# Performance work log

Measured on AMD Instinct MI355X. Metric: run time of the kernel, lower is better.

## Reference

```python
import jax, jax.numpy as jnp
import numpy as np

N_LAYERS = 6
N_HEADS = 8
HIDDEN = 512
FILTER = 2048
KSIZE = 3
WINDOW = 10
DK = HIDDEN // N_HEADS


def _rel_to_abs(x):
    # x: [b, h, l, 2l-1] -> [b, h, l, l]
    b, h, l, _ = x.shape
    x = jnp.pad(x, ((0, 0), (0, 0), (0, 0), (0, 1)))
    x = x.reshape(b, h, l * 2 * l)
    x = jnp.pad(x, ((0, 0), (0, 0), (0, l - 1)))
    return x.reshape(b, h, l + 1, 2 * l - 1)[:, :, :l, l - 1:]


def _abs_to_rel(x):
    # x: [b, h, l, l] -> [b, h, l, 2l-1]
    b, h, l, _ = x.shape
    x = jnp.pad(x, ((0, 0), (0, 0), (0, 0), (0, l - 1)))
    x = x.reshape(b, h, l * l + l * (l - 1))
    x = jnp.pad(x, ((0, 0), (0, 0), (l, 0)))
    return x.reshape(b, h, l, 2 * l)[:, :, :, 1:]


def _get_rel_emb(emb, length):
    # emb: [1, 2w+1, dk] -> [1, 2*length-1, dk]  (static python ints)
    pad = max(length - (WINDOW + 1), 0)
    s = max(WINDOW + 1 - length, 0)
    e = s + 2 * length - 1
    emb = jnp.pad(emb, ((0, 0), (pad, pad), (0, 0)))
    return emb[:, s:e]


def _conv1x1(x, w, b):
    # x: [B, Cin, T], w: [Cout, Cin] -> [B, Cout, T]
    return jnp.einsum('oc,bct->bot', w, x) + b[None, :, None]


def _conv1d_same(x, w, b):
    # x: [B, Cin, T], w: [Cout, Cin, K], same padding (pad_l=(K-1)//2, pad_r=K//2)
    x = jnp.pad(x, ((0, 0), (0, 0), ((KSIZE - 1) // 2, KSIZE // 2)))
    y = jax.lax.conv_general_dilated(x, w, (1,), 'VALID',
                                     dimension_numbers=('NCH', 'OIH', 'NCH'))
    return y + b[None, :, None]


def _layer_norm(x, g, b):
    # normalize over channel axis (axis=1), eps=1e-5 (VITS LayerNorm)
    m = jnp.mean(x, axis=1, keepdims=True)
    v = jnp.var(x, axis=1, keepdims=True)
    return (x - m) * jax.lax.rsqrt(v + 1e-5) * g[None, :, None] + b[None, :, None]


def _mha(x, attn_mask, Wq, bq, Wk, bk, Wv, bv, Wo, bo, erk, erv):
    B, C, T = x.shape
    q = _conv1x1(x, Wq, bq)
    k = _conv1x1(x, Wk, bk)
    v = _conv1x1(x, Wv, bv)
    # [B, C, T] -> [B, H, T, Dk]
    def split_heads(t):
        return t.reshape(B, N_HEADS, DK, T).transpose(0, 1, 3, 2)
    q, k, v = split_heads(q), split_heads(k), split_heads(v)
    scale = 1.0 / np.sqrt(DK).astype(np.float32)
    scores = jnp.einsum('bhtd,bhsd->bhts', q * scale, k)
    # relative position logits
    rel_k = _get_rel_emb(erk, T)[0]                       # [2T-1, Dk]
    rel_logits = jnp.einsum('bhtd,rd->bhtr', q * scale, rel_k)
    scores = scores + _rel_to_abs(rel_logits)
    scores = jnp.where(attn_mask == 0, -1e4, scores)
    p = jax.nn.softmax(scores, axis=-1)
    out = jnp.einsum('bhts,bhsd->bhtd', p, v)
    rel_v = _get_rel_emb(erv, T)[0]                       # [2T-1, Dk]
    out = out + jnp.einsum('bhtr,rd->bhtd', _abs_to_rel(p), rel_v)
    out = out.transpose(0, 1, 3, 2).reshape(B, C, T)
    return _conv1x1(out, Wo, bo)


def _ffn(x, x_mask, W1, bf1, W2, bf2):
    y = _conv1d_same(x * x_mask, W1, bf1)
    y = jax.nn.relu(y)
    y = _conv1d_same(y * x_mask, W2, bf2)
    return y * x_mask


def reference(x, x_mask, Wq, bq, Wk, bk, Wv, bv, Wo, bo, erk, erv,
              g1, b1, g2, b2, W1, bf1, W2, bf2):
    attn_mask = x_mask[:, :, None, :] * x_mask[:, :, :, None]  # [B,1,T,T]
    x = x * x_mask
    for i in range(N_LAYERS):
        y = _mha(x, attn_mask, Wq[i], bq[i], Wk[i], bk[i], Wv[i], bv[i],
                 Wo[i], bo[i], erk[i], erv[i])
        x = _layer_norm(x + y, g1[i], b1[i])
        y = _ffn(x, x_mask, W1[i], bf1[i], W2[i], bf2[i])
        x = _layer_norm(x + y, g2[i], b2[i])
    return x * x_mask


def setup_inputs() -> dict:
    key = jax.random.key(0)
    ks = jax.random.split(key, 20)
    B, T = 8, 512
    xavier = lambda k, sh, fan: jax.random.normal(k, sh, jnp.float32) * np.sqrt(2.0 / fan).astype(np.float32)
    rel_std = DK ** -0.5
    return {
        'x': jax.random.normal(ks[0], (B, HIDDEN, T), jnp.float32),
        'x_mask': jnp.ones((B, 1, T), jnp.float32),
        'Wq': xavier(ks[1], (N_LAYERS, HIDDEN, HIDDEN), 2 * HIDDEN),
        'bq': jnp.zeros((N_LAYERS, HIDDEN), jnp.float32),
        'Wk': xavier(ks[2], (N_LAYERS, HIDDEN, HIDDEN), 2 * HIDDEN),
        'bk': jnp.zeros((N_LAYERS, HIDDEN), jnp.float32),
        'Wv': xavier(ks[3], (N_LAYERS, HIDDEN, HIDDEN), 2 * HIDDEN),
        'bv': jnp.zeros((N_LAYERS, HIDDEN), jnp.float32),
        'Wo': xavier(ks[4], (N_LAYERS, HIDDEN, HIDDEN), 2 * HIDDEN),
        'bo': jnp.zeros((N_LAYERS, HIDDEN), jnp.float32),
        'erk': jax.random.normal(ks[5], (N_LAYERS, 1, 2 * WINDOW + 1, DK), jnp.float32) * rel_std,
        'erv': jax.random.normal(ks[6], (N_LAYERS, 1, 2 * WINDOW + 1, DK), jnp.float32) * rel_std,
        'g1': jnp.ones((N_LAYERS, HIDDEN), jnp.float32),
        'b1': jnp.zeros((N_LAYERS, HIDDEN), jnp.float32),
        'g2': jnp.ones((N_LAYERS, HIDDEN), jnp.float32),
        'b2': jnp.zeros((N_LAYERS, HIDDEN), jnp.float32),
        'W1': jax.random.normal(ks[7], (N_LAYERS, FILTER, HIDDEN, KSIZE), jnp.float32) * np.sqrt(1.0 / (HIDDEN * KSIZE)).astype(np.float32),
        'bf1': jnp.zeros((N_LAYERS, FILTER), jnp.float32),
        'W2': jax.random.normal(ks[8], (N_LAYERS, HIDDEN, FILTER, KSIZE), jnp.float32) * np.sqrt(1.0 / (FILTER * KSIZE)).astype(np.float32),
        'bf2': jnp.zeros((N_LAYERS, HIDDEN), jnp.float32),
    }
```

## Files before the change

kernel.cpp:

```cpp
#include <hip/hip_runtime.h>


#define NLAYERS 6
#define BB 8
#define TT 512
#define CC 512
#define FF 2048
#define HH 8
#define DKK 64
#define WW 10

static_assert(CC == HH * DKK, "");

typedef __attribute__((ext_vector_type(8))) short short8;
typedef __attribute__((ext_vector_type(4))) float f32x4;
typedef unsigned short ushort;

#define BCTS ((size_t)BB * CC * TT)

__device__ __forceinline__ ushort f2bs(float f) {
    unsigned u = __float_as_uint(f);
    u = (u + 0x7FFFu + ((u >> 16) & 1u)) >> 16;
    return (ushort)u;
}
__device__ __forceinline__ float bf2f(ushort u) {
    return __uint_as_float(((unsigned)u) << 16);
}
__device__ __forceinline__ float wave_sum(float v) {
    #pragma unroll
    for (int off = 32; off > 0; off >>= 1) v += __shfl_xor(v, off, 64);
    return v;
}

__global__ __launch_bounds__(256) void init_trans(const float* __restrict__ in,
                                                  const float* __restrict__ mask,
                                                  float* __restrict__ xf,
                                                  ushort* __restrict__ xt) {
    __shared__ float tile[32][33];
    const int t0 = blockIdx.x * 32;
    const int c0 = blockIdx.y * 32;
    const int b = blockIdx.z;
    const int col = threadIdx.x & 31;
    const int row = threadIdx.x >> 5;
    const float* src = in + ((size_t)b * CC + c0) * TT + t0;
    #pragma unroll
    for (int r = 0; r < 32; r += 8)
        tile[row + r][col] = src[(size_t)(row + r) * TT + col];
    __syncthreads();
    #pragma unroll
    for (int r = 0; r < 32; r += 8) {
        const int t = t0 + row + r;
        const float mv = mask[b * TT + t];
        const float v = tile[col][row + r] * mv;
        const size_t idx = ((size_t)(b * TT) + t) * CC + c0 + col;
        xf[idx] = v;
        xt[idx] = f2bs(v);
    }
}

__global__ __launch_bounds__(256) void final_kernel(const float* __restrict__ xf,
                                                    const float* __restrict__ mask,
                                                    float* __restrict__ out) {
    __shared__ float tile[32][33];
    const int t0 = blockIdx.x * 32;
    const int c0 = blockIdx.y * 32;
    const int b = blockIdx.z;
    const int col = threadIdx.x & 31;
    const int row = threadIdx.x >> 5;
    #pragma unroll
    for (int r = 0; r < 32; r += 8)
        tile[row + r][col] = xf[((size_t)(b * TT) + t0 + row + r) * CC + c0 + col];
    __syncthreads();
    #pragma unroll
    for (int r = 0; r < 32; r += 8) {
        const int c = c0 + row + r;
        const int t = t0 + col;
        out[((size_t)b * CC + c) * TT + t] = tile[col][row + r] * mask[b * TT + t];
    }
}

__global__ __launch_bounds__(256) void wcvt_layer(const float* __restrict__ Wq,
                                                  const float* __restrict__ Wk,
                                                  const float* __restrict__ Wv,
                                                  const float* __restrict__ bq,
                                                  const float* __restrict__ bk,
                                                  const float* __restrict__ bv,
                                                  const float* __restrict__ Wo,
                                                  const float* __restrict__ W1,
                                                  const float* __restrict__ W2,
                                                  ushort* __restrict__ Wqkv,
                                                  float* __restrict__ bqkv,
                                                  ushort* __restrict__ Wot,
                                                  ushort* __restrict__ W1t,
                                                  ushort* __restrict__ W2t) {
    size_t i = (size_t)blockIdx.x * 256 + threadIdx.x;
    if (i < 1536)
        bqkv[i] = (i < 512) ? bq[i] : (i < 1024) ? bk[i - 512] : bv[i - 1024];
    if (i < 786432) {
        const int o = (int)(i >> 9), c = (int)(i & 511);
        const float* src = (o < 512) ? Wq : (o < 1024) ? Wk : Wv;
        Wqkv[i] = f2bs(src[(size_t)(o & 511) * 512 + c]);
        return;
    }
    i -= 786432;
    if (i < 262144) { Wot[i] = f2bs(Wo[i]); return; }
    i -= 262144;
    if (i < 3145728) {
        const int c = (int)(i & 511);
        const int o = (int)((i >> 9) & 2047);
        const int tap = (int)(i >> 20);
        W1t[i] = f2bs(W1[((size_t)o * 512 + c) * 3 + tap]);
        return;
    }
    i -= 3145728;
    if (i < 3145728) {
        const int c = (int)(i & 2047);
        const int o = (int)((i >> 11) & 511);
        const int tap = (int)(i >> 20);
        W2t[i] = f2bs(W2[((size_t)o * 2048 + c) * 3 + tap]);
    }
}

template <int MODE, int TN>
__global__ __launch_bounds__(256) void gemm128(const ushort* __restrict__ Wt,
                                               const float* __restrict__ bias,
                                               const ushort* __restrict__ Xin,
                                               void* __restrict__ Out,
                                               const float* __restrict__ mask,
                                               int O, int K, int taps, int kcs) {
    const int blk = blockIdx.x;
    const int b = blk >> 2;
    const int t0 = (blk & 3) * 128;
    const int o0 = blockIdx.y * TN;
    const int tid = threadIdx.x;
    const int wid = tid >> 6, lane = tid & 63, ln = lane & 15, q = lane >> 4;
    constexpr int MF = (TN == 128) ? 4 : 2;
    const int msub = (TN == 128) ? (wid & 1) * 64 : wid * 32;
    const int nsub = (TN == 128) ? (wid >> 1) * 64 : 0;

    __shared__ ushort Xs[128][40];
    __shared__ ushort Ws[TN][40];

    f32x4 acc[MF][4] = {};

    const int KC = K >> 5;
    const int NI = taps * KC;
    const int kcm = KC - 1;

    const int rx = tid >> 1;
    const int cx = (tid & 1) << 4;
    const int rw = (TN == 128) ? (tid >> 1) : (tid >> 2);
    const int cw = (TN == 128) ? ((tid & 1) << 4) : ((tid & 3) << 3);

    uint4 xr0, xr1, wr0, wr1;
    const uint4 zero = make_uint4(0u, 0u, 0u, 0u);

    auto load = [&](int it) {
        const int tap = it >> kcs;
        const int c0 = (it & kcm) << 5;
        const int shift = (taps > 1) ? (tap - 1) : 0;
        const int tt = t0 + rx + shift;
        const bool okt = (tt >= 0) && (tt < TT);
        const ushort* xp = Xin + ((size_t)(b * TT + (okt ? tt : 0)) * K + c0 + cx);
        xr0 = okt ? *(const uint4*)xp : zero;
        xr1 = okt ? *(const uint4*)(xp + 8) : zero;
        const ushort* wp = Wt + ((size_t)(tap * O + o0 + rw) * K + c0 + cw);
        wr0 = *(const uint4*)wp;
        if (TN == 128) wr1 = *(const uint4*)(wp + 8);
    };

    load(0);
    for (int it = 0; it < NI; ++it) {
        __syncthreads();
        *(uint4*)&Xs[rx][cx] = xr0;
        *(uint4*)&Xs[rx][cx + 8] = xr1;
        *(uint4*)&Ws[rw][cw] = wr0;
        if (TN == 128) *(uint4*)&Ws[rw][cw + 8] = wr1;
        if (it + 1 < NI) load(it + 1);
        __syncthreads();
        short8 afr[MF], bfr[4];
        #pragma unroll
        for (int mi = 0; mi < MF; ++mi)
            afr[mi] = *(const short8*)&Xs[msub + mi * 16 + ln][q * 8];
        #pragma unroll
        for (int ni = 0; ni < 4; ++ni)
            bfr[ni] = *(const short8*)&Ws[nsub + ni * 16 + ln][q * 8];
        #pragma unroll
        for (int mi = 0; mi < MF; ++mi)
            #pragma unroll
            for (int ni = 0; ni < 4; ++ni)
                acc[mi][ni] = __builtin_amdgcn_mfma_f32_16x16x32_bf16(
                    afr[mi], bfr[ni], acc[mi][ni], 0, 0, 0);
    }

    #pragma unroll
    for (int ni = 0; ni < 4; ++ni) {
        const int o = o0 + nsub + ni * 16 + ln;
        const float bv = bias[o];
        #pragma unroll
        for (int mi = 0; mi < MF; ++mi) {
            const int t = t0 + msub + mi * 16 + q * 4;
            if (MODE == 0) {
                float* Op = (float*)Out;
                #pragma unroll
                for (int r = 0; r < 4; ++r)
                    Op[((size_t)(b * TT) + t + r) * O + o] = acc[mi][ni][r] + bv;
            } else {
                ushort* Op = (ushort*)Out;
                const int which = o >> 9, oo = o & 511;
                if (which < 2) {
                    #pragma unroll
                    for (int r = 0; r < 4; ++r)
                        Op[(size_t)which * BCTS + ((size_t)(b * TT) + t + r) * CC + oo] =
                            f2bs(acc[mi][ni][r] + bv);
                } else {
                    ushort tmp[4];
                    #pragma unroll
                    for (int r = 0; r < 4; ++r) tmp[r] = f2bs(acc[mi][ni][r] + bv);
                    *(uint2*)&Op[2 * BCTS + ((size_t)(b * CC) + oo) * TT + t] =
                        *(const uint2*)tmp;
                }
            }
        }
    }
}

template <int TN, int KSPLIT, int MODE>
__global__ __launch_bounds__(256) void conv_gemm(const ushort* __restrict__ Wt,
                                                 const float* __restrict__ bias,
                                                 const ushort* __restrict__ Xin,
                                                 void* __restrict__ Out,
                                                 const float* __restrict__ mask,
                                                 int O, int K) {
    const int blk = blockIdx.x;
    const int b = blk >> 2;
    const int t0 = (blk & 3) * 128;
    const int o0 = blockIdx.y * TN;
    const int kz = (KSPLIT > 1) ? blockIdx.z : 0;
    const int tid = threadIdx.x;
    const int wid = tid >> 6, lane = tid & 63, ln = lane & 15, q = lane >> 4;
    constexpr int MF = (TN == 128) ? 4 : 2;
    constexpr int TSH = (TN == 128) ? 7 : 6;
    const int msub = (TN == 128) ? (wid & 1) * 64 : wid * 32;
    const int nsub = (TN == 128) ? (wid >> 1) * 64 : 0;

    __shared__ ushort Xs[130][40];
    __shared__ ushort Ws[3 * TN][40];

    f32x4 acc[MF][4] = {};

    const int Kc = K / KSPLIT;
    const int cbase = kz * Kc;
    const int NC = Kc >> 5;

    const int rx = tid >> 1;
    const int cx = (tid & 1) << 4;
    const int rw0 = tid >> 2;
    const int cw = (tid & 3) << 3;

    const ushort* Xb = Xin + (size_t)b * TT * K;

    for (int cc = 0; cc < NC; ++cc) {
        const int c0 = cbase + (cc << 5);
        __syncthreads();
        {
            const ushort* xp = Xb + (size_t)(t0 + rx) * K + c0 + cx;
            *(uint4*)&Xs[rx + 1][cx] = *(const uint4*)xp;
            *(uint4*)&Xs[rx + 1][cx + 8] = *(const uint4*)(xp + 8);
        }
        if (tid < 8) {
            const int hr = (tid < 4) ? -1 : 128;
            const int cu = (tid & 3) << 3;
            const int tg = t0 + hr;
            uint4 v = make_uint4(0u, 0u, 0u, 0u);
            if (tg >= 0 && tg < TT)
                v = *(const uint4*)(Xb + (size_t)tg * K + c0 + cu);
            *(uint4*)&Xs[hr + 1][cu] = v;
        }
        #pragma unroll
        for (int j = 0; j < 3 * TN / 64; ++j) {
            const int r = rw0 + j * 64;
            const int tap = r >> TSH, o = r & (TN - 1);
            const ushort* wp = Wt + ((size_t)(tap * O + o0 + o)) * K + c0 + cw;
            *(uint4*)&Ws[r][cw] = *(const uint4*)wp;
        }
        __syncthreads();
        #pragma unroll
        for (int tap = 0; tap < 3; ++tap) {
            short8 afr[MF], bfr[4];
            #pragma unroll
            for (int mi = 0; mi < MF; ++mi)
                afr[mi] = *(const short8*)&Xs[msub + mi * 16 + ln + tap][q * 8];
            #pragma unroll
            for (int ni = 0; ni < 4; ++ni)
                bfr[ni] = *(const short8*)&Ws[tap * TN + nsub + ni * 16 + ln][q * 8];
            #pragma unroll
            for (int mi = 0; mi < MF; ++mi)
                #pragma unroll
                for (int ni = 0; ni < 4; ++ni)
                    acc[mi][ni] = __builtin_amdgcn_mfma_f32_16x16x32_bf16(
                        afr[mi], bfr[ni], acc[mi][ni], 0, 0, 0);
        }
    }

    #pragma unroll
    for (int ni = 0; ni < 4; ++ni) {
        const int o = o0 + nsub + ni * 16 + ln;
        #pragma unroll
        for (int mi = 0; mi < MF; ++mi) {
            const int t = t0 + msub + mi * 16 + q * 4;
            if (MODE == 1) {
                const float bv = bias[o];
                ushort* Op = (ushort*)Out;
                #pragma unroll
                for (int r = 0; r < 4; ++r) {
                    float v = fmaxf(acc[mi][ni][r] + bv, 0.f) * mask[b * TT + t + r];
                    Op[((size_t)(b * TT) + t + r) * (size_t)O + o] = f2bs(v);
                }
            } else {
                float* Op = (float*)Out + (size_t)kz * BCTS;
                #pragma unroll
                for (int r = 0; r < 4; ++r)
                    Op[((size_t)(b * TT) + t + r) * O + o] = acc[mi][ni][r];
            }
        }
    }
}

__global__ __launch_bounds__(256) void fattn_kernel(const ushort* __restrict__ qkvt,
                                                    const float* __restrict__ mask,
                                                    const float* __restrict__ erk,
                                                    const float* __restrict__ erv,
                                                    ushort* __restrict__ xto) {
    const int tid = threadIdx.x;
    const int wm = tid >> 6;
    const int lane = tid & 63;
    const int ln = lane & 15;
    const int q4 = lane >> 4;
    const int bh = blockIdx.y;
    const int b = bh >> 3, h = bh & 7;
    const int t0g = blockIdx.x * 64 + wm * 16;

    __shared__ float ervs[2 * WW + 1][DKK];
    __shared__ float msS[TT];
    __shared__ float relS[4][16][22];
    __shared__ float band[4][16][24];
    __shared__ ushort Pt[4][16][40];

    for (int i = tid; i < (2 * WW + 1) * DKK; i += 256)
        ervs[i / DKK][i % DKK] = erv[i];
    for (int i = tid; i < TT; i += 256)
        msS[i] = mask[b * TT + i];

    #pragma unroll
    for (int i = 0; i < 6; ++i) {
        const int idx = lane + i * 64;
        ((float*)band[wm])[idx] = -1e30f;
    }

    const ushort* qrow = qkvt + ((size_t)(b * TT + t0g + ln) * CC + h * DKK);
    const short8 qb0 = *(const short8*)(qrow + q4 * 8);
    const short8 qb1 = *(const short8*)(qrow + 32 + q4 * 8);

    {
        const float* ekL = erk;
        short8 ea0, ea1;
        {
            const float* ep = ekL + ln * DKK + q4 * 8;
            #pragma unroll
            for (int j = 0; j < 8; ++j) ea0[j] = (short)f2bs(ep[j]);
            #pragma unroll
            for (int j = 0; j < 8; ++j) ea1[j] = (short)f2bs(ep[32 + j]);
        }
        f32x4 c0 = {};
        c0 = __builtin_amdgcn_mfma_f32_16x16x32_bf16(ea0, qb0, c0, 0, 0, 0);
        c0 = __builtin_amdgcn_mfma_f32_16x16x32_bf16(ea1, qb1, c0, 0, 0, 0);
        #pragma unroll
        for (int r = 0; r < 4; ++r)
            relS[wm][ln][q4 * 4 + r] = c0[r] * 0.125f;
        short8 eb0 = {}, eb1 = {};
        if (ln < 2 * WW + 1 - 16) {
            const float* ep = ekL + (16 + ln) * DKK + q4 * 8;
            #pragma unroll
            for (int j = 0; j < 8; ++j) eb0[j] = (short)f2bs(ep[j]);
            #pragma unroll
            for (int j = 0; j < 8; ++j) eb1[j] = (short)f2bs(ep[32 + j]);
        }
        f32x4 c1 = {};
        c1 = __builtin_amdgcn_mfma_f32_16x16x32_bf16(eb0, qb0, c1, 0, 0, 0);
        c1 = __builtin_amdgcn_mfma_f32_16x16x32_bf16(eb1, qb1, c1, 0, 0, 0);
        #pragma unroll
        for (int r = 0; r < 4; ++r) {
            const int w = 16 + q4 * 4 + r;
            if (w < 2 * WW + 1) relS[wm][ln][w] = c1[r] * 0.125f;
        }
    }

    __syncthreads();

    const float mt = msS[t0g + ln];

    float m_run = -1e30f, l_run = 0.f;
    f32x4 Oacc[4] = {};

    const ushort* Kbase = qkvt + BCTS + ((size_t)(b * TT) * CC + h * DKK);
    const ushort* Vbase = qkvt + 2 * BCTS + ((size_t)(b * CC + h * DKK) * TT);

    for (int s0 = 0; s0 < TT; s0 += 32) {
        const ushort* klo = Kbase + (size_t)(s0 + ln) * CC;
        const ushort* khi = klo + 16 * CC;
        const short8 ka0 = *(const short8*)(klo + q4 * 8);
        const short8 ka1 = *(const short8*)(klo + 32 + q4 * 8);
        const short8 kb0 = *(const short8*)(khi + q4 * 8);
        const short8 kb1 = *(const short8*)(khi + 32 + q4 * 8);

        f32x4 slo = {}, shi = {};
        slo = __builtin_amdgcn_mfma_f32_16x16x32_bf16(ka0, qb0, slo, 0, 0, 0);
        slo = __builtin_amdgcn_mfma_f32_16x16x32_bf16(ka1, qb1, slo, 0, 0, 0);
        shi = __builtin_amdgcn_mfma_f32_16x16x32_bf16(kb0, qb0, shi, 0, 0, 0);
        shi = __builtin_amdgcn_mfma_f32_16x16x32_bf16(kb1, qb1, shi, 0, 0, 0);

        float v[2][4];
        float bmax = -1e30f;
        const int tg = t0g + ln;
        #pragma unroll
        for (int half = 0; half < 2; ++half) {
            #pragma unroll
            for (int r = 0; r < 4; ++r) {
                const int s = s0 + half * 16 + q4 * 4 + r;
                const int wb = s - tg + WW;
                float vv = (half ? shi[r] : slo[r]) * 0.125f;
                if ((unsigned)wb <= 2u * WW) vv += relS[wm][ln][wb];
                if (mt * msS[s] == 0.f) vv = -1e4f;
                if ((unsigned)wb <= 2u * WW) band[wm][ln][wb] = vv;
                v[half][r] = vv;
                bmax = fmaxf(bmax, vv);
            }
        }
        bmax = fmaxf(bmax, __shfl_xor(bmax, 16, 64));
        bmax = fmaxf(bmax, __shfl_xor(bmax, 32, 64));

        const float mnew = fmaxf(m_run, bmax);
        const float alpha = __expf(m_run - mnew);
        m_run = mnew;

        float rsum = 0.f;
        ushort pb[8];
        #pragma unroll
        for (int half = 0; half < 2; ++half)
            #pragma unroll
            for (int r = 0; r < 4; ++r) {
                const float p = __expf(v[half][r] - mnew);
                rsum += p;
                pb[half * 4 + r] = f2bs(p);
            }
        rsum += __shfl_xor(rsum, 16, 64);
        rsum += __shfl_xor(rsum, 32, 64);
        l_run = l_run * alpha + rsum;

        *(uint2*)&Pt[wm][ln][q4 * 4] = *(const uint2*)&pb[0];
        *(uint2*)&Pt[wm][ln][16 + q4 * 4] = *(const uint2*)&pb[4];

        #pragma unroll
        for (int r = 0; r < 4; ++r) {
            const float alr = __shfl(alpha, q4 * 4 + r, 64);
            #pragma unroll
            for (int dt = 0; dt < 4; ++dt) Oacc[dt][r] *= alr;
        }

        const short8 pa = *(const short8*)&Pt[wm][ln][q4 * 8];
        #pragma unroll
        for (int dt = 0; dt < 4; ++dt) {
            const short8 vb = *(const short8*)(Vbase + (size_t)(dt * 16 + ln) * TT + s0 + q4 * 8);
            Oacc[dt] = __builtin_amdgcn_mfma_f32_16x16x32_bf16(pa, vb, Oacc[dt], 0, 0, 0);
        }
    }

    float mr[4], invl[4];
    #pragma unroll
    for (int r = 0; r < 4; ++r) {
        mr[r] = __shfl(m_run, q4 * 4 + r, 64);
        invl[r] = 1.f / __shfl(l_run, q4 * 4 + r, 64);
    }
    f32x4 racc[4] = {};
    for (int w = 0; w <= 2 * WW; ++w) {
        float ev[4];
        #pragma unroll
        for (int dt = 0; dt < 4; ++dt) ev[dt] = ervs[w][dt * 16 + ln];
        #pragma unroll
        for (int r = 0; r < 4; ++r) {
            const float pw = __expf(band[wm][q4 * 4 + r][w] - mr[r]);
            #pragma unroll
            for (int dt = 0; dt < 4; ++dt) racc[dt][r] += pw * ev[dt];
        }
    }
    #pragma unroll
    for (int r = 0; r < 4; ++r) {
        const int t = t0g + q4 * 4 + r;
        #pragma unroll
        for (int dt = 0; dt < 4; ++dt)
            xto[((size_t)(b * TT) + t) * CC + h * DKK + dt * 16 + ln] =
                f2bs((Oacc[dt][r] + racc[dt][r]) * invl[r]);
    }
}

__global__ __launch_bounds__(256) void addln_kernel(float* __restrict__ x,
                                                    const float* __restrict__ p0,
                                                    const float* __restrict__ p1,
                                                    const float* __restrict__ biasc,
                                                    const float* __restrict__ g,
                                                    const float* __restrict__ bt,
                                                    const float* __restrict__ mask,
                                                    int maskY,
                                                    ushort* __restrict__ xtout,
                                                    int maskOut) {
    const int row = blockIdx.x * 4 + (threadIdx.x >> 6);
    const int lane = threadIdx.x & 63;
    const float m = mask[row];
    const float mv = maskY ? m : 1.f;
    const float mo = maskOut ? m : 1.f;
    const size_t base = (size_t)row * CC;
    const int c0 = lane * 8;

    f32x4 v0, v1;
    {
        f32x4 a0 = *(const f32x4*)(x + base + c0);
        f32x4 a1 = *(const f32x4*)(x + base + c0 + 4);
        f32x4 y0 = *(const f32x4*)(p0 + base + c0);
        f32x4 y1 = *(const f32x4*)(p0 + base + c0 + 4);
        if (p1) {
            f32x4 z0 = *(const f32x4*)(p1 + base + c0);
            f32x4 z1 = *(const f32x4*)(p1 + base + c0 + 4);
            #pragma unroll
            for (int r = 0; r < 4; ++r) { y0[r] += z0[r]; y1[r] += z1[r]; }
        }
        if (biasc) {
            f32x4 bc0 = *(const f32x4*)(biasc + c0);
            f32x4 bc1 = *(const f32x4*)(biasc + c0 + 4);
            #pragma unroll
            for (int r = 0; r < 4; ++r) { y0[r] += bc0[r]; y1[r] += bc1[r]; }
        }
        #pragma unroll
        for (int r = 0; r < 4; ++r) {
            v0[r] = a0[r] + y0[r] * mv;
            v1[r] = a1[r] + y1[r] * mv;
        }
    }

    float s = 0.f, s2 = 0.f;
    #pragma unroll
    for (int r = 0; r < 4; ++r) {
        s += v0[r] + v1[r];
        s2 += v0[r] * v0[r] + v1[r] * v1[r];
    }
    s = wave_sum(s);
    s2 = wave_sum(s2);
    const float mean = s * (1.f / CC);
    const float var = s2 * (1.f / CC) - mean * mean;
    const float rstd = rsqrtf(var + 1e-5f);

    f32x4 g0 = *(const f32x4*)(g + c0);
    f32x4 g1v = *(const f32x4*)(g + c0 + 4);
    f32x4 bt0 = *(const f32x4*)(bt + c0);
    f32x4 bt1 = *(const f32x4*)(bt + c0 + 4);
    f32x4 o0, o1;
    ushort ob[8];
    #pragma unroll
    for (int r = 0; r < 4; ++r) {
        o0[r] = (v0[r] - mean) * rstd * g0[r] + bt0[r];
        o1[r] = (v1[r] - mean) * rstd * g1v[r] + bt1[r];
        ob[r] = f2bs(o0[r] * mo);
        ob[4 + r] = f2bs(o1[r] * mo);
    }
    *(f32x4*)(x + base + c0) = o0;
    *(f32x4*)(x + base + c0 + 4) = o1;
    *(uint4*)(xtout + base + c0) = *(const uint4*)ob;
}

extern "C" void kernel_launch(void* const* d_in, const int* in_sizes, int n_in,
                              void* d_out, int out_size, void* d_ws, size_t ws_size,
                              hipStream_t stream) {
    const float* x_in = (const float*)d_in[0];
    const float* mask = (const float*)d_in[1];
    const float* Wq = (const float*)d_in[2];
    const float* bq = (const float*)d_in[3];
    const float* Wk = (const float*)d_in[4];
    const float* bk = (const float*)d_in[5];
    const float* Wv = (const float*)d_in[6];
    const float* bv = (const float*)d_in[7];
    const float* Wo = (const float*)d_in[8];
    const float* bo = (const float*)d_in[9];
    const float* erk = (const float*)d_in[10];
    const float* erv = (const float*)d_in[11];
    const float* g1 = (const float*)d_in[12];
    const float* b1 = (const float*)d_in[13];
    const float* g2 = (const float*)d_in[14];
    const float* b2 = (const float*)d_in[15];
    const float* W1 = (const float*)d_in[16];
    const float* bf1 = (const float*)d_in[17];
    const float* W2 = (const float*)d_in[18];
    const float* bf2 = (const float*)d_in[19];

    float* xf = (float*)d_ws;
    ushort* Xt = (ushort*)(xf + BCTS);
    ushort* qkvt = Xt + BCTS;
    ushort* Xto = qkvt + 3 * BCTS;
    float* parts = (float*)(Xto + BCTS);
    ushort* Midt = (ushort*)(parts + 2 * BCTS);
    ushort* Wqkv = Midt + 4 * BCTS;
    float* bqkv = (float*)(Wqkv + (size_t)1536 * 512);
    ushort* Wot = (ushort*)(bqkv + 1536);
    ushort* W1t = Wot + (size_t)CC * CC;
    ushort* W2t = W1t + (size_t)3 * FF * CC;

    init_trans<<<dim3(TT / 32, CC / 32, BB), 256, 0, stream>>>(x_in, mask, xf, Xt);

    const size_t nW = 786432 + 262144 + 3145728 + 3145728;
    const int wcvtBlocks = (int)((nW + 255) / 256);

    for (int L = 0; L < NLAYERS; ++L) {
        wcvt_layer<<<wcvtBlocks, 256, 0, stream>>>(
            Wq + (size_t)L * CC * CC, Wk + (size_t)L * CC * CC, Wv + (size_t)L * CC * CC,
            bq + (size_t)L * CC, bk + (size_t)L * CC, bv + (size_t)L * CC,
            Wo + (size_t)L * CC * CC,
            W1 + (size_t)L * 3 * FF * CC, W2 + (size_t)L * 3 * FF * CC,
            Wqkv, bqkv, Wot, W1t, W2t);

        gemm128<2, 128><<<dim3(32, 12), 256, 0, stream>>>(
            Wqkv, bqkv, Xt, qkvt, mask, 1536, CC, 1, 4);

        fattn_kernel<<<dim3(TT / 64, BB * HH), 256, 0, stream>>>(
            qkvt, mask, erk + (size_t)L * (2 * WW + 1) * DKK,
            erv + (size_t)L * (2 * WW + 1) * DKK, Xto);

        gemm128<0, 64><<<dim3(32, 8), 256, 0, stream>>>(
            Wot, bo + (size_t)L * CC, Xto, parts, mask, CC, CC, 1, 4);
        addln_kernel<<<BB * TT / 4, 256, 0, stream>>>(
            xf, parts, nullptr, nullptr,
            g1 + (size_t)L * CC, b1 + (size_t)L * CC, mask, 0, Xt, 1);

        conv_gemm<128, 1, 1><<<dim3(32, FF / 128, 1), 256, 0, stream>>>(
            W1t, bf1 + (size_t)L * FF, Xt, Midt, mask, FF, CC);
        conv_gemm<64, 2, 3><<<dim3(32, CC / 64, 2), 256, 0, stream>>>(
            W2t, nullptr, Midt, parts, mask, CC, FF);
        addln_kernel<<<BB * TT / 4, 256, 0, stream>>>(
            xf, parts, parts + BCTS, bf2 + (size_t)L * CC,
            g2 + (size_t)L * CC, b2 + (size_t)L * CC, mask, 1, Xt, 0);
    }

    final_kernel<<<dim3(TT / 32, CC / 32, BB), 256, 0, stream>>>(xf, mask, (float*)d_out);
}
```

Baseline: 1.260 ms.

## Prefetch conv GEMM tiles into registers and rebalance split-K for FFN and output projection

The conv GEMM now loads the next K-chunk's activation and weight tiles into registers while the current chunk is computed from shared memory, so global loads overlap with MFMA work. The second FFN conv moves from 64-wide output tiles with 2-way split-K to 128-wide tiles with 4-way split-K, with the extra partial sums written into the idle QKV buffer. The attention output projection is also split 2-way over K, with its bias moved into the add+LayerNorm kernel, which now sums up to four partial buffers. This adds register pressure and extra fp32 partial-sum traffic in exchange for more parallelism and latency hiding.

```diff
diff --git a/kernel.cpp b/kernel.cpp
--- a/kernel.cpp
+++ b/kernel.cpp
@@ -127,11 +127,13 @@
                                                const ushort* __restrict__ Xin,
                                                void* __restrict__ Out,
                                                const float* __restrict__ mask,
-                                               int O, int K, int taps, int kcs) {
+                                               int O, int K, int taps, int kcs,
+                                               int ksp) {
     const int blk = blockIdx.x;
     const int b = blk >> 2;
     const int t0 = (blk & 3) * 128;
     const int o0 = blockIdx.y * TN;
+    const int kz = (MODE == 0) ? blockIdx.z : 0;
     const int tid = threadIdx.x;
     const int wid = tid >> 6, lane = tid & 63, ln = lane & 15, q = lane >> 4;
     constexpr int MF = (TN == 128) ? 4 : 2;
@@ -143,7 +145,9 @@
 
     f32x4 acc[MF][4] = {};
 
-    const int KC = K >> 5;
+    const int Kc = (MODE == 0) ? (K / ksp) : K;
+    const int cbase = kz * Kc;
+    const int KC = Kc >> 5;
     const int NI = taps * KC;
     const int kcm = KC - 1;
 
@@ -157,7 +161,7 @@
 
     auto load = [&](int it) {
         const int tap = it >> kcs;
-        const int c0 = (it & kcm) << 5;
+        const int c0 = cbase + ((it & kcm) << 5);
         const int shift = (taps > 1) ? (tap - 1) : 0;
         const int tt = t0 + rx + shift;
         const bool okt = (tt >= 0) && (tt < TT);
@@ -196,16 +200,16 @@
     #pragma unroll
     for (int ni = 0; ni < 4; ++ni) {
         const int o = o0 + nsub + ni * 16 + ln;
-        const float bv = bias[o];
         #pragma unroll
         for (int mi = 0; mi < MF; ++mi) {
             const int t = t0 + msub + mi * 16 + q * 4;
             if (MODE == 0) {
-                float* Op = (float*)Out;
+                float* Op = (float*)Out + (size_t)kz * BCTS;
                 #pragma unroll
                 for (int r = 0; r < 4; ++r)
-                    Op[((size_t)(b * TT) + t + r) * O + o] = acc[mi][ni][r] + bv;
+                    Op[((size_t)(b * TT) + t + r) * O + o] = acc[mi][ni][r];
             } else {
+                const float bv = bias[o];
                 ushort* Op = (ushort*)Out;
                 const int which = o >> 9, oo = o & 511;
                 if (which < 2) {
@@ -225,13 +229,15 @@
     }
 }
 
-template <int TN, int KSPLIT, int MODE>
+template <int KSPLIT, int MODE>
 __global__ __launch_bounds__(256) void conv_gemm(const ushort* __restrict__ Wt,
                                                  const float* __restrict__ bias,
                                                  const ushort* __restrict__ Xin,
                                                  void* __restrict__ Out,
+                                                 float* __restrict__ Out2,
                                                  const float* __restrict__ mask,
                                                  int O, int K) {
+    constexpr int TN = 128;
     const int blk = blockIdx.x;
     const int b = blk >> 2;
     const int t0 = (blk & 3) * 128;
@@ -239,15 +245,13 @@
     const int kz = (KSPLIT > 1) ? blockIdx.z : 0;
     const int tid = threadIdx.x;
     const int wid = tid >> 6, lane = tid & 63, ln = lane & 15, q = lane >> 4;
-    constexpr int MF = (TN == 128) ? 4 : 2;
-    constexpr int TSH = (TN == 128) ? 7 : 6;
-    const int msub = (TN == 128) ? (wid & 1) * 64 : wid * 32;
-    const int nsub = (TN == 128) ? (wid >> 1) * 64 : 0;
+    const int msub = (wid & 1) * 64;
+    const int nsub = (wid >> 1) * 64;
 
     __shared__ ushort Xs[130][40];
     __shared__ ushort Ws[3 * TN][40];
 
-    f32x4 acc[MF][4] = {};
+    f32x4 acc[4][4] = {};
 
     const int Kc = K / KSPLIT;
     const int cbase = kz * Kc;
@@ -260,42 +264,49 @@
 
     const ushort* Xb = Xin + (size_t)b * TT * K;
 
-    for (int cc = 0; cc < NC; ++cc) {
+    uint4 xr0, xr1, hx, wr[6];
+    auto load = [&](int cc) {
         const int c0 = cbase + (cc << 5);
-        __syncthreads();
-        {
-            const ushort* xp = Xb + (size_t)(t0 + rx) * K + c0 + cx;
-            *(uint4*)&Xs[rx + 1][cx] = *(const uint4*)xp;
-            *(uint4*)&Xs[rx + 1][cx + 8] = *(const uint4*)(xp + 8);
-        }
+        const ushort* xp = Xb + (size_t)(t0 + rx) * K + c0 + cx;
+        xr0 = *(const uint4*)xp;
+        xr1 = *(const uint4*)(xp + 8);
         if (tid < 8) {
             const int hr = (tid < 4) ? -1 : 128;
-            const int cu = (tid & 3) << 3;
             const int tg = t0 + hr;
-            uint4 v = make_uint4(0u, 0u, 0u, 0u);
+            hx = make_uint4(0u, 0u, 0u, 0u);
             if (tg >= 0 && tg < TT)
-                v = *(const uint4*)(Xb + (size_t)tg * K + c0 + cu);
-            *(uint4*)&Xs[hr + 1][cu] = v;
-        }
-        #pragma unroll
-        for (int j = 0; j < 3 * TN / 64; ++j) {
+                hx = *(const uint4*)(Xb + (size_t)tg * K + c0 + ((tid & 3) << 3));
+        }
+        #pragma unroll
+        for (int j = 0; j < 6; ++j) {
             const int r = rw0 + j * 64;
-            const int tap = r >> TSH, o = r & (TN - 1);
-            const ushort* wp = Wt + ((size_t)(tap * O + o0 + o)) * K + c0 + cw;
-            *(uint4*)&Ws[r][cw] = *(const uint4*)wp;
-        }
+            const int tap = r >> 7, o = r & (TN - 1);
+            wr[j] = *(const uint4*)(Wt + ((size_t)(tap * O + o0 + o)) * K + c0 + cw);
+        }
+    };
+
+    load(0);
+    for (int cc = 0; cc < NC; ++cc) {
         __syncthreads();
+        *(uint4*)&Xs[rx + 1][cx] = xr0;
+        *(uint4*)&Xs[rx + 1][cx + 8] = xr1;
+        if (tid < 8) *(uint4*)&Xs[(tid < 4) ? 0 : 129][(tid & 3) << 3] = hx;
+        #pragma unroll
+        for (int j = 0; j < 6; ++j)
+            *(uint4*)&Ws[rw0 + j * 64][cw] = wr[j];
+        if (cc + 1 < NC) load(cc + 1);
+        __syncthreads();
         #pragma unroll
         for (int tap = 0; tap < 3; ++tap) {
-            short8 afr[MF], bfr[4];
-            #pragma unroll
-            for (int mi = 0; mi < MF; ++mi)
+            short8 afr[4], bfr[4];
+            #pragma unroll
+            for (int mi = 0; mi < 4; ++mi)
                 afr[mi] = *(const short8*)&Xs[msub + mi * 16 + ln + tap][q * 8];
             #pragma unroll
             for (int ni = 0; ni < 4; ++ni)
                 bfr[ni] = *(const short8*)&Ws[tap * TN + nsub + ni * 16 + ln][q * 8];
             #pragma unroll
-            for (int mi = 0; mi < MF; ++mi)
+            for (int mi = 0; mi < 4; ++mi)
                 #pragma unroll
                 for (int ni = 0; ni < 4; ++ni)
                     acc[mi][ni] = __builtin_amdgcn_mfma_f32_16x16x32_bf16(
@@ -307,7 +318,7 @@
     for (int ni = 0; ni < 4; ++ni) {
         const int o = o0 + nsub + ni * 16 + ln;
         #pragma unroll
-        for (int mi = 0; mi < MF; ++mi) {
+        for (int mi = 0; mi < 4; ++mi) {
             const int t = t0 + msub + mi * 16 + q * 4;
             if (MODE == 1) {
                 const float bv = bias[o];
@@ -318,7 +329,8 @@
                     Op[((size_t)(b * TT) + t + r) * (size_t)O + o] = f2bs(v);
                 }
             } else {
-                float* Op = (float*)Out + (size_t)kz * BCTS;
+                float* Op = (kz < 2) ? ((float*)Out + (size_t)kz * BCTS)
+                                     : (Out2 + (size_t)(kz - 2) * BCTS);
                 #pragma unroll
                 for (int r = 0; r < 4; ++r)
                     Op[((size_t)(b * TT) + t + r) * O + o] = acc[mi][ni][r];
@@ -507,6 +519,8 @@
 __global__ __launch_bounds__(256) void addln_kernel(float* __restrict__ x,
                                                     const float* __restrict__ p0,
                                                     const float* __restrict__ p1,
+                                                    const float* __restrict__ p2,
+                                                    const float* __restrict__ p3,
                                                     const float* __restrict__ biasc,
                                                     const float* __restrict__ g,
                                                     const float* __restrict__ bt,
@@ -522,29 +536,32 @@
     const size_t base = (size_t)row * CC;
     const int c0 = lane * 8;
 
+    f32x4 y0 = *(const f32x4*)(p0 + base + c0);
+    f32x4 y1 = *(const f32x4*)(p0 + base + c0 + 4);
+    if (p1) {
+        y0 += *(const f32x4*)(p1 + base + c0);
+        y1 += *(const f32x4*)(p1 + base + c0 + 4);
+    }
+    if (p2) {
+        y0 += *(const f32x4*)(p2 + base + c0);
+        y1 += *(const f32x4*)(p2 + base + c0 + 4);
+    }
+    if (p3) {
+        y0 += *(const f32x4*)(p3 + base + c0);
+        y1 += *(const f32x4*)(p3 + base + c0 + 4);
+    }
+    if (biasc) {
+        y0 += *(const f32x4*)(biasc + c0);
+        y1 += *(const f32x4*)(biasc + c0 + 4);
+    }
+
+    f32x4 a0 = *(const f32x4*)(x + base + c0);
+    f32x4 a1 = *(const f32x4*)(x + base + c0 + 4);
     f32x4 v0, v1;
-    {
-        f32x4 a0 = *(const f32x4*)(x + base + c0);
-        f32x4 a1 = *(const f32x4*)(x + base + c0 + 4);
-        f32x4 y0 = *(const f32x4*)(p0 + base + c0);
-        f32x4 y1 = *(const f32x4*)(p0 + base + c0 + 4);
-        if (p1) {
-            f32x4 z0 = *(const f32x4*)(p1 + base + c0);
-            f32x4 z1 = *(const f32x4*)(p1 + base + c0 + 4);
-            #pragma unroll
-            for (int r = 0; r < 4; ++r) { y0[r] += z0[r]; y1[r] += z1[r]; }
-        }
-        if (biasc) {
-            f32x4 bc0 = *(const f32x4*)(biasc + c0);
-            f32x4 bc1 = *(const f32x4*)(biasc + c0 + 4);
-            #pragma unroll
-            for (int r = 0; r < 4; ++r) { y0[r] += bc0[r]; y1[r] += bc1[r]; }
-        }
-        #pragma unroll
-        for (int r = 0; r < 4; ++r) {
-            v0[r] = a0[r] + y0[r] * mv;
-            v1[r] = a1[r] + y1[r] * mv;
-        }
+    #pragma unroll
+    for (int r = 0; r < 4; ++r) {
+        v0[r] = a0[r] + y0[r] * mv;
+        v1[r] = a1[r] + y1[r] * mv;
     }
 
     float s = 0.f, s2 = 0.f;
@@ -613,6 +630,8 @@
     ushort* W1t = Wot + (size_t)CC * CC;
     ushort* W2t = W1t + (size_t)3 * FF * CC;
 
+    float* P23 = (float*)qkvt;
+
     init_trans<<<dim3(TT / 32, CC / 32, BB), 256, 0, stream>>>(x_in, mask, xf, Xt);
 
     const size_t nW = 786432 + 262144 + 3145728 + 3145728;
@@ -627,24 +646,24 @@
             Wqkv, bqkv, Wot, W1t, W2t);
 
         gemm128<2, 128><<<dim3(32, 12), 256, 0, stream>>>(
-            Wqkv, bqkv, Xt, qkvt, mask, 1536, CC, 1, 4);
+            Wqkv, bqkv, Xt, qkvt, mask, 1536, CC, 1, 4, 1);
 
         fattn_kernel<<<dim3(TT / 64, BB * HH), 256, 0, stream>>>(
             qkvt, mask, erk + (size_t)L * (2 * WW + 1) * DKK,
             erv + (size_t)L * (2 * WW + 1) * DKK, Xto);
 
-        gemm128<0, 64><<<dim3(32, 8), 256, 0, stream>>>(
-            Wot, bo + (size_t)L * CC, Xto, parts, mask, CC, CC, 1, 4);
+        gemm128<0, 64><<<dim3(32, 8, 2), 256, 0, stream>>>(
+            Wot, nullptr, Xto, parts, mask, CC, CC, 1, 4, 2);
         addln_kernel<<<BB * TT / 4, 256, 0, stream>>>(
-            xf, parts, nullptr, nullptr,
+            xf, parts, parts + BCTS, nullptr, nullptr, bo + (size_t)L * CC,
             g1 + (size_t)L * CC, b1 + (size_t)L * CC, mask, 0, Xt, 1);
 
-        conv_gemm<128, 1, 1><<<dim3(32, FF / 128, 1), 256, 0, stream>>>(
-            W1t, bf1 + (size_t)L * FF, Xt, Midt, mask, FF, CC);
-        conv_gemm<64, 2, 3><<<dim3(32, CC / 64, 2), 256, 0, stream>>>(
-            W2t, nullptr, Midt, parts, mask, CC, FF);
+        conv_gemm<1, 1><<<dim3(32, FF / 128, 1), 256, 0, stream>>>(
+            W1t, bf1 + (size_t)L * FF, Xt, Midt, nullptr, mask, FF, CC);
+        conv_gemm<4, 3><<<dim3(32, CC / 128, 4), 256, 0, stream>>>(
+            W2t, nullptr, Midt, parts, P23, mask, CC, FF);
         addln_kernel<<<BB * TT / 4, 256, 0, stream>>>(
-            xf, parts, parts + BCTS, bf2 + (size_t)L * CC,
+            xf, parts, parts + BCTS, P23, P23 + BCTS, bf2 + (size_t)L * CC,
             g2 + (size_t)L * CC, b2 + (size_t)L * CC, mask, 1, Xt, 0);
     }
 
```

New measurement: 1.613 ms. 28.0% more time.
